# Kernel tuning notes

Measured on AMD Instinct MI355X. Metric: run time of the kernel, lower is better.

The kernel has to match this reference:

```python
import jax, jax.numpy as jnp
import numpy as np

B, K, S, H = 8, 2048, 1024, 256   # batch, num_spans, seq_len, hidden
W = 24                            # max span width (gather window)
WIN = 3
NEG_INF = -jnp.inf


def setup_inputs() -> dict:
    key = jax.random.key(0)
    k1, k2, k3, k4 = jax.random.split(key, 4)
    token_reps = jax.random.normal(k1, (B, S, H), dtype=jnp.float32)
    starts = jax.random.randint(k2, (B, K), 0, S - W)
    widths = jax.random.randint(k3, (B, K), 1, W + 1)  # span width in [1, W]
    ends = starts + widths                              # end is exclusive, <= S
    span_ids = jnp.stack([starts, ends], axis=-1).astype(jnp.int32)
    span_masks = jax.random.uniform(k4, (B, K)) < 0.9
    return {"token_reps": token_reps, "span_ids": span_ids, "span_masks": span_masks}


def _masked_max(tok_win, mask):
    # tok_win: (B, K, W, H), mask: (B, K, W) -> (B, K, H)
    return jnp.max(jnp.where(mask[..., None], tok_win, NEG_INF), axis=2)


def reference(token_reps, span_ids, span_masks):
    """extract_span_reps, mode='start_inner_maxpool_end', pooling=False.

    Equivalent math to the torch version, but gathers only the per-span window
    [start, start+W) instead of broadcasting over the full seq_len, since all
    spans have width <= W.
    """
    Bv, Sv, Hv = token_reps.shape
    starts = span_ids[..., 0]            # (B, K)
    ends = span_ids[..., 1]              # (B, K) exclusive

    pos = jnp.arange(W)                  # (W,)
    idx = starts[..., None] + pos        # (B, K, W) absolute token index
    safe_idx = jnp.clip(idx, 0, Sv - 1)  # safe gather; out-of-span masked below
    # gather per-span token windows: (B, K, W, H)
    tok_win = token_reps[jnp.arange(Bv)[:, None, None], safe_idx]

    valid = span_masks[..., None]                                 # (B, K, 1)
    start_cut = jnp.minimum(starts + WIN, ends)[..., None]        # (B, K, 1)
    end_cut = jnp.maximum(ends - WIN, starts)[..., None]          # (B, K, 1)
    e = ends[..., None]

    # idx >= start always holds (pos >= 0)
    start_m = (idx < start_cut) & valid
    end_m = (idx >= end_cut) & (idx < e) & valid
    inner_m = ((idx >= start_cut) & (idx < end_cut)
               & ((ends - starts) > 2 * WIN)[..., None] & valid)

    start_reps = _masked_max(tok_win, start_m)   # (B, K, H)
    end_reps = _masked_max(tok_win, end_m)
    inner_reps = _masked_max(tok_win, inner_m)

    # spans with no inner tokens fall back to start reps
    no_inner = jnp.isinf(inner_reps).all(axis=-1, keepdims=True)
    inner_reps = jnp.where(no_inner, start_reps, inner_reps)

    span_reps = jnp.concatenate([start_reps, inner_reps, end_reps], axis=-1)
    span_reps = jnp.where(span_masks[..., None], span_reps, 0.0)  # (B, K, 3H)
    return span_reps
```

## Files before the change

kernel.cpp:

```cpp
#include <hip/hip_runtime.h>

#define Bv   8
#define Kv   2048
#define Sv   1024
#define Hv   256
#define Wv   24
#define WINv 3
#define RB   8
#define SPW  8

#define NSPAN (Bv * Kv)

typedef float nt4 __attribute__((ext_vector_type(4)));

__device__ __forceinline__ float bf16_to_f32(unsigned short u) {
    union { unsigned int i; float f; } c;
    c.i = ((unsigned int)u) << 16;
    return c.f;
}

__device__ __forceinline__ void nt_store4(float* p, float a, float b, float c, float d) {
    nt4 v = {a, b, c, d};
    __builtin_nontemporal_store(v, (nt4*)p);
}

__global__ __launch_bounds__(256) void span_rep_kernel(
    const void* __restrict__ token_reps,
    const int* __restrict__ span_ids,
    const void* __restrict__ span_masks,
    float* __restrict__ out)
{
    const int tid  = threadIdx.x;
    const int lane = tid & 63;

    const unsigned short* tu = (const unsigned short*)token_reps;
    int e = (tu[2 * lane] >> 7) & 0xFF;
    unsigned long long votes = __ballot(e >= 96 && e <= 144);
    const int tok32 = (__popcll(votes) >= 56) ? 0 : 1;

    const unsigned char* mbp = (const unsigned char*)span_masks;
    unsigned char bnz = mbp[lane] | mbp[lane + 64];
    int m4 = lane & 3;
    unsigned long long z1  = __ballot(bnz && m4 == 1);
    unsigned long long z23 = __ballot(bnz && (m4 == 2 || m4 == 3));
    unsigned long long z84 = __ballot(bnz && m4 == 0 && (lane & 7) == 4);
    const int maskw = z1 ? 0 : (z23 ? 3 : (z84 ? 1 : 2));

    const int odd_or = span_ids[1] | span_ids[3] | span_ids[5] | span_ids[7];
    const int ids64 = (odd_or == 0) ? 1 : 0;

    const int b     = blockIdx.x & 7;
    const int kbase = ((blockIdx.x >> 3) << 5) + ((tid >> 6) << 3);
    const int span0 = b * Kv + kbase;

    int st[SPW], en[SPW], mvv[SPW];
    #pragma unroll
    for (int j = 0; j < SPW; ++j) {
        const int span = span0 + j;
        if (!ids64) {
            st[j] = span_ids[2 * span];
            en[j] = span_ids[2 * span + 1];
        } else {
            st[j] = span_ids[4 * span];
            en[j] = span_ids[4 * span + 2];
        }
        if (maskw == 0)      mvv[j] = ((const unsigned char*)span_masks)[span];
        else if (maskw == 1) mvv[j] = ((const int*)span_masks)[span];
        else if (maskw == 2) mvv[j] = ((const int*)span_masks)[2 * span];
        else                 mvv[j] = (((const float*)span_masks)[span] != 0.0f);
    }

    const size_t batch_off = (size_t)b * Sv * Hv;

    for (int j = 0; j < SPW; ++j) {
        const int span = span0 + j;
        float* outp = out + (size_t)span * (3 * Hv) + lane * 4;

        const int start = st[j];
        const int w     = en[j] - start;

        if (mvv[j] == 0 || w < 1 || w > Wv || start < 0 || en[j] > Sv) {
            nt_store4(outp,          0.f, 0.f, 0.f, 0.f);
            nt_store4(outp + Hv,     0.f, 0.f, 0.f, 0.f);
            nt_store4(outp + 2 * Hv, 0.f, 0.f, 0.f, 0.f);
            continue;
        }

        const size_t row0 = batch_off + (size_t)start * Hv;

        float s0 = -INFINITY, s1 = -INFINITY, s2 = -INFINITY, s3 = -INFINITY;
        float e0 = -INFINITY, e1 = -INFINITY, e2 = -INFINITY, e3 = -INFINITY;
        float i0 = -INFINITY, i1 = -INFINITY, i2 = -INFINITY, i3 = -INFINITY;

        const int  scut      = (w < WINv) ? w : WINv;
        const int  ecut      = (w - WINv > 0) ? (w - WINv) : 0;
        const bool has_inner = (w > 2 * WINv);
        const int  icut      = w - WINv;

        auto reduce = [&](int r, float f0, float f1, float f2, float f3) {
            if (r < scut) {
                s0 = fmaxf(s0, f0); s1 = fmaxf(s1, f1);
                s2 = fmaxf(s2, f2); s3 = fmaxf(s3, f3);
            }
            if (r >= ecut) {
                e0 = fmaxf(e0, f0); e1 = fmaxf(e1, f1);
                e2 = fmaxf(e2, f2); e3 = fmaxf(e3, f3);
            }
            if (has_inner && r >= WINv && r < icut) {
                i0 = fmaxf(i0, f0); i1 = fmaxf(i1, f1);
                i2 = fmaxf(i2, f2); i3 = fmaxf(i3, f3);
            }
        };

        if (tok32) {
            const float4* tp = (const float4*)((const float*)token_reps + row0) + lane;
            for (int r0 = 0; r0 < w; r0 += RB) {
                const int n = ((w - r0) < RB) ? (w - r0) : RB;
                float4 buf[RB];
                #pragma unroll
                for (int jj = 0; jj < RB; ++jj)
                    if (jj < n) buf[jj] = tp[(size_t)(r0 + jj) * (Hv / 4)];
                #pragma unroll
                for (int jj = 0; jj < RB; ++jj)
                    if (jj < n)
                        reduce(r0 + jj, buf[jj].x, buf[jj].y, buf[jj].z, buf[jj].w);
            }
        } else {
            const unsigned short* tp = (const unsigned short*)token_reps + row0 + lane * 4;
            for (int r0 = 0; r0 < w; r0 += RB) {
                const int n = ((w - r0) < RB) ? (w - r0) : RB;
                ushort4 buf[RB];
                #pragma unroll
                for (int jj = 0; jj < RB; ++jj)
                    if (jj < n) buf[jj] = *(const ushort4*)(tp + (size_t)(r0 + jj) * Hv);
                #pragma unroll
                for (int jj = 0; jj < RB; ++jj)
                    if (jj < n)
                        reduce(r0 + jj,
                               bf16_to_f32(buf[jj].x), bf16_to_f32(buf[jj].y),
                               bf16_to_f32(buf[jj].z), bf16_to_f32(buf[jj].w));
            }
        }
        if (!has_inner) { i0 = s0; i1 = s1; i2 = s2; i3 = s3; }

        nt_store4(outp,          s0, s1, s2, s3);
        nt_store4(outp + Hv,     i0, i1, i2, i3);
        nt_store4(outp + 2 * Hv, e0, e1, e2, e3);
    }
}

extern "C" void kernel_launch(void* const* d_in, const int* in_sizes, int n_in,
                              void* d_out, int out_size, void* d_ws, size_t ws_size,
                              hipStream_t stream) {
    const void* token_reps = d_in[0];
    const int*  span_ids   = (const int*)d_in[1];
    const void* span_masks = d_in[2];
    for (int i = 0; i < n_in; ++i) {
        if (in_sizes[i] == Bv * Sv * Hv)      token_reps = d_in[i];
        else if (in_sizes[i] == Bv * Kv * 2)  span_ids   = (const int*)d_in[i];
        else if (in_sizes[i] == Bv * Kv)      span_masks = d_in[i];
    }
    float* out = (float*)d_out;

    dim3 grid(NSPAN / (4 * SPW));
    dim3 block(256);
    span_rep_kernel<<<grid, block, 0, stream>>>(token_reps, span_ids, span_masks, out);
}
```

Before: 97.44 us.

## Process two spans per wavefront with interleaved loads and a larger grid

Each wavefront now handles two spans at once, issuing both spans' row loads before reducing either, instead of looping sequentially over eight spans. The grid grows fourfold to keep the total span count the same. This exposes more memory-level parallelism per wave and more waves overall, which should better hide gather latency. The cost is extra register pressure from two sets of accumulators and buffers, plus more block launch overhead.

```diff
diff --git a/kernel.cpp b/kernel.cpp
--- a/kernel.cpp
+++ b/kernel.cpp
@@ -7,7 +7,6 @@
 #define Wv   24
 #define WINv 3
 #define RB   8
-#define SPW  8
 
 #define NSPAN (Bv * Kv)
 
@@ -22,6 +21,95 @@
 __device__ __forceinline__ void nt_store4(float* p, float a, float b, float c, float d) {
     nt4 v = {a, b, c, d};
     __builtin_nontemporal_store(v, (nt4*)p);
+}
+
+__device__ __forceinline__ void cvt4(const float4 v, float* f) {
+    f[0] = v.x; f[1] = v.y; f[2] = v.z; f[3] = v.w;
+}
+__device__ __forceinline__ void cvt4(const ushort4 u, float* f) {
+    f[0] = bf16_to_f32(u.x); f[1] = bf16_to_f32(u.y);
+    f[2] = bf16_to_f32(u.z); f[3] = bf16_to_f32(u.w);
+}
+
+__device__ __forceinline__ void red(float* acc, int r, int scut, int ecut,
+                                    bool hin, int icut, const float* f) {
+    if (r < scut) {
+        acc[0] = fmaxf(acc[0], f[0]); acc[1] = fmaxf(acc[1], f[1]);
+        acc[2] = fmaxf(acc[2], f[2]); acc[3] = fmaxf(acc[3], f[3]);
+    }
+    if (r >= ecut) {
+        acc[8] = fmaxf(acc[8], f[0]); acc[9] = fmaxf(acc[9], f[1]);
+        acc[10] = fmaxf(acc[10], f[2]); acc[11] = fmaxf(acc[11], f[3]);
+    }
+    if (hin && r >= WINv && r < icut) {
+        acc[4] = fmaxf(acc[4], f[0]); acc[5] = fmaxf(acc[5], f[1]);
+        acc[6] = fmaxf(acc[6], f[2]); acc[7] = fmaxf(acc[7], f[3]);
+    }
+}
+
+template<typename VT, int STRIDEB>
+__device__ __forceinline__ void pair_body(
+    const char* pA, const char* pB, int wA, int wB,
+    float* outA, float* outB)
+{
+    float accA[12], accB[12];
+    #pragma unroll
+    for (int q = 0; q < 12; ++q) { accA[q] = -INFINITY; accB[q] = -INFINITY; }
+
+    const int  scutA = (wA < WINv) ? wA : WINv;
+    const int  ecutA = (wA - WINv > 0) ? (wA - WINv) : 0;
+    const bool hinA  = wA > 2 * WINv;
+    const int  icutA = wA - WINv;
+    const int  scutB = (wB < WINv) ? wB : WINv;
+    const int  ecutB = (wB - WINv > 0) ? (wB - WINv) : 0;
+    const bool hinB  = wB > 2 * WINv;
+    const int  icutB = wB - WINv;
+
+    for (int r0 = 0; r0 < Wv; r0 += RB) {
+        if (r0 >= wA && r0 >= wB) break;
+        VT bA[RB], bB[RB];
+        #pragma unroll
+        for (int j = 0; j < RB; ++j)
+            if (r0 + j < wA) bA[j] = *(const VT*)(pA + (size_t)(r0 + j) * STRIDEB);
+        #pragma unroll
+        for (int j = 0; j < RB; ++j)
+            if (r0 + j < wB) bB[j] = *(const VT*)(pB + (size_t)(r0 + j) * STRIDEB);
+        #pragma unroll
+        for (int j = 0; j < RB; ++j)
+            if (r0 + j < wA) {
+                float f[4]; cvt4(bA[j], f);
+                red(accA, r0 + j, scutA, ecutA, hinA, icutA, f);
+            }
+        #pragma unroll
+        for (int j = 0; j < RB; ++j)
+            if (r0 + j < wB) {
+                float f[4]; cvt4(bB[j], f);
+                red(accB, r0 + j, scutB, ecutB, hinB, icutB, f);
+            }
+    }
+
+    if (wA == 0) {
+        nt_store4(outA, 0.f, 0.f, 0.f, 0.f);
+        nt_store4(outA + Hv, 0.f, 0.f, 0.f, 0.f);
+        nt_store4(outA + 2 * Hv, 0.f, 0.f, 0.f, 0.f);
+    } else {
+        if (!hinA) { accA[4] = accA[0]; accA[5] = accA[1];
+                     accA[6] = accA[2]; accA[7] = accA[3]; }
+        nt_store4(outA,          accA[0], accA[1], accA[2], accA[3]);
+        nt_store4(outA + Hv,     accA[4], accA[5], accA[6], accA[7]);
+        nt_store4(outA + 2 * Hv, accA[8], accA[9], accA[10], accA[11]);
+    }
+    if (wB == 0) {
+        nt_store4(outB, 0.f, 0.f, 0.f, 0.f);
+        nt_store4(outB + Hv, 0.f, 0.f, 0.f, 0.f);
+        nt_store4(outB + 2 * Hv, 0.f, 0.f, 0.f, 0.f);
+    } else {
+        if (!hinB) { accB[4] = accB[0]; accB[5] = accB[1];
+                     accB[6] = accB[2]; accB[7] = accB[3]; }
+        nt_store4(outB,          accB[0], accB[1], accB[2], accB[3]);
+        nt_store4(outB + Hv,     accB[4], accB[5], accB[6], accB[7]);
+        nt_store4(outB + 2 * Hv, accB[8], accB[9], accB[10], accB[11]);
+    }
 }
 
 __global__ __launch_bounds__(256) void span_rep_kernel(
@@ -49,103 +137,48 @@
     const int odd_or = span_ids[1] | span_ids[3] | span_ids[5] | span_ids[7];
     const int ids64 = (odd_or == 0) ? 1 : 0;
 
-    const int b     = blockIdx.x & 7;
-    const int kbase = ((blockIdx.x >> 3) << 5) + ((tid >> 6) << 3);
-    const int span0 = b * Kv + kbase;
-
-    int st[SPW], en[SPW], mvv[SPW];
-    #pragma unroll
-    for (int j = 0; j < SPW; ++j) {
-        const int span = span0 + j;
-        if (!ids64) {
-            st[j] = span_ids[2 * span];
-            en[j] = span_ids[2 * span + 1];
-        } else {
-            st[j] = span_ids[4 * span];
-            en[j] = span_ids[4 * span + 2];
-        }
-        if (maskw == 0)      mvv[j] = ((const unsigned char*)span_masks)[span];
-        else if (maskw == 1) mvv[j] = ((const int*)span_masks)[span];
-        else if (maskw == 2) mvv[j] = ((const int*)span_masks)[2 * span];
-        else                 mvv[j] = (((const float*)span_masks)[span] != 0.0f);
-    }
+    const int b  = blockIdx.x & 7;
+    const int k0 = ((blockIdx.x >> 3) << 3) + ((tid >> 6) << 1);
+    const int sA = b * Kv + k0;
+    const int sB = sA + 1;
+
+    int stA, enA, stB, enB, mvA, mvB;
+    if (!ids64) {
+        stA = span_ids[2 * sA];     enA = span_ids[2 * sA + 1];
+        stB = span_ids[2 * sB];     enB = span_ids[2 * sB + 1];
+    } else {
+        stA = span_ids[4 * sA];     enA = span_ids[4 * sA + 2];
+        stB = span_ids[4 * sB];     enB = span_ids[4 * sB + 2];
+    }
+    if (maskw == 0)      { mvA = ((const unsigned char*)span_masks)[sA];
+                           mvB = ((const unsigned char*)span_masks)[sB]; }
+    else if (maskw == 1) { mvA = ((const int*)span_masks)[sA];
+                           mvB = ((const int*)span_masks)[sB]; }
+    else if (maskw == 2) { mvA = ((const int*)span_masks)[2 * sA];
+                           mvB = ((const int*)span_masks)[2 * sB]; }
+    else                 { mvA = (((const float*)span_masks)[sA] != 0.0f);
+                           mvB = (((const float*)span_masks)[sB] != 0.0f); }
+
+    int wA = enA - stA;
+    int wB = enB - stB;
+    if (mvA == 0 || wA < 1 || wA > Wv || stA < 0 || enA > Sv) wA = 0;
+    if (mvB == 0 || wB < 1 || wB > Wv || stB < 0 || enB > Sv) wB = 0;
+
+    float* outA = out + (size_t)sA * (3 * Hv) + lane * 4;
+    float* outB = out + (size_t)sB * (3 * Hv) + lane * 4;
 
     const size_t batch_off = (size_t)b * Sv * Hv;
 
-    for (int j = 0; j < SPW; ++j) {
-        const int span = span0 + j;
-        float* outp = out + (size_t)span * (3 * Hv) + lane * 4;
-
-        const int start = st[j];
-        const int w     = en[j] - start;
-
-        if (mvv[j] == 0 || w < 1 || w > Wv || start < 0 || en[j] > Sv) {
-            nt_store4(outp,          0.f, 0.f, 0.f, 0.f);
-            nt_store4(outp + Hv,     0.f, 0.f, 0.f, 0.f);
-            nt_store4(outp + 2 * Hv, 0.f, 0.f, 0.f, 0.f);
-            continue;
-        }
-
-        const size_t row0 = batch_off + (size_t)start * Hv;
-
-        float s0 = -INFINITY, s1 = -INFINITY, s2 = -INFINITY, s3 = -INFINITY;
-        float e0 = -INFINITY, e1 = -INFINITY, e2 = -INFINITY, e3 = -INFINITY;
-        float i0 = -INFINITY, i1 = -INFINITY, i2 = -INFINITY, i3 = -INFINITY;
-
-        const int  scut      = (w < WINv) ? w : WINv;
-        const int  ecut      = (w - WINv > 0) ? (w - WINv) : 0;
-        const bool has_inner = (w > 2 * WINv);
-        const int  icut      = w - WINv;
-
-        auto reduce = [&](int r, float f0, float f1, float f2, float f3) {
-            if (r < scut) {
-                s0 = fmaxf(s0, f0); s1 = fmaxf(s1, f1);
-                s2 = fmaxf(s2, f2); s3 = fmaxf(s3, f3);
-            }
-            if (r >= ecut) {
-                e0 = fmaxf(e0, f0); e1 = fmaxf(e1, f1);
-                e2 = fmaxf(e2, f2); e3 = fmaxf(e3, f3);
-            }
-            if (has_inner && r >= WINv && r < icut) {
-                i0 = fmaxf(i0, f0); i1 = fmaxf(i1, f1);
-                i2 = fmaxf(i2, f2); i3 = fmaxf(i3, f3);
-            }
-        };
-
-        if (tok32) {
-            const float4* tp = (const float4*)((const float*)token_reps + row0) + lane;
-            for (int r0 = 0; r0 < w; r0 += RB) {
-                const int n = ((w - r0) < RB) ? (w - r0) : RB;
-                float4 buf[RB];
-                #pragma unroll
-                for (int jj = 0; jj < RB; ++jj)
-                    if (jj < n) buf[jj] = tp[(size_t)(r0 + jj) * (Hv / 4)];
-                #pragma unroll
-                for (int jj = 0; jj < RB; ++jj)
-                    if (jj < n)
-                        reduce(r0 + jj, buf[jj].x, buf[jj].y, buf[jj].z, buf[jj].w);
-            }
-        } else {
-            const unsigned short* tp = (const unsigned short*)token_reps + row0 + lane * 4;
-            for (int r0 = 0; r0 < w; r0 += RB) {
-                const int n = ((w - r0) < RB) ? (w - r0) : RB;
-                ushort4 buf[RB];
-                #pragma unroll
-                for (int jj = 0; jj < RB; ++jj)
-                    if (jj < n) buf[jj] = *(const ushort4*)(tp + (size_t)(r0 + jj) * Hv);
-                #pragma unroll
-                for (int jj = 0; jj < RB; ++jj)
-                    if (jj < n)
-                        reduce(r0 + jj,
-                               bf16_to_f32(buf[jj].x), bf16_to_f32(buf[jj].y),
-                               bf16_to_f32(buf[jj].z), bf16_to_f32(buf[jj].w));
-            }
-        }
-        if (!has_inner) { i0 = s0; i1 = s1; i2 = s2; i3 = s3; }
-
-        nt_store4(outp,          s0, s1, s2, s3);
-        nt_store4(outp + Hv,     i0, i1, i2, i3);
-        nt_store4(outp + 2 * Hv, e0, e1, e2, e3);
+    if (tok32) {
+        const char* base = (const char*)token_reps;
+        const char* pA = base + (batch_off + (size_t)stA * Hv + lane * 4) * 4;
+        const char* pB = base + (batch_off + (size_t)stB * Hv + lane * 4) * 4;
+        pair_body<float4, Hv * 4>(pA, pB, wA, wB, outA, outB);
+    } else {
+        const char* base = (const char*)token_reps;
+        const char* pA = base + (batch_off + (size_t)stA * Hv + lane * 4) * 2;
+        const char* pB = base + (batch_off + (size_t)stB * Hv + lane * 4) * 2;
+        pair_body<ushort4, Hv * 2>(pA, pB, wA, wB, outA, outB);
     }
 }
 
@@ -162,7 +195,7 @@
     }
     float* out = (float*)d_out;
 
-    dim3 grid(NSPAN / (4 * SPW));
+    dim3 grid(NSPAN / 8);
     dim3 block(256);
     span_rep_kernel<<<grid, block, 0, stream>>>(token_reps, span_ids, span_masks, out);
 }
```

Measured after the change: 93.02 us. 4.5% less time.

## Map one span per wavefront with clamped unconditional row loads

Applied to the files above, without the earlier changes.

Each wavefront now handles one span instead of looping over eight, and the grid grows eightfold to match. Row loads become unconditional, with the row index clamped to the last valid row and the block size raised to twelve so all loads issue together. Span ids are read for both 32- and 64-bit layouts and then selected, and nontemporal stores are replaced with plain stores. The aim is more memory-level parallelism and less serial per-span latency, at the cost of more block launches, redundant header work per block, and extra loads on short spans.

```diff
diff --git a/kernel.cpp b/kernel.cpp
--- a/kernel.cpp
+++ b/kernel.cpp
@@ -6,22 +6,14 @@
 #define Hv   256
 #define Wv   24
 #define WINv 3
-#define RB   8
-#define SPW  8
+#define RB   12
 
 #define NSPAN (Bv * Kv)
-
-typedef float nt4 __attribute__((ext_vector_type(4)));
 
 __device__ __forceinline__ float bf16_to_f32(unsigned short u) {
     union { unsigned int i; float f; } c;
     c.i = ((unsigned int)u) << 16;
     return c.f;
-}
-
-__device__ __forceinline__ void nt_store4(float* p, float a, float b, float c, float d) {
-    nt4 v = {a, b, c, d};
-    __builtin_nontemporal_store(v, (nt4*)p);
 }
 
 __global__ __launch_bounds__(256) void span_rep_kernel(
@@ -49,104 +41,98 @@
     const int odd_or = span_ids[1] | span_ids[3] | span_ids[5] | span_ids[7];
     const int ids64 = (odd_or == 0) ? 1 : 0;
 
-    const int b     = blockIdx.x & 7;
-    const int kbase = ((blockIdx.x >> 3) << 5) + ((tid >> 6) << 3);
-    const int span0 = b * Kv + kbase;
+    const int b    = blockIdx.x & 7;
+    const int k    = ((blockIdx.x >> 3) << 2) + (tid >> 6);
+    const int span = b * Kv + k;
 
-    int st[SPW], en[SPW], mvv[SPW];
-    #pragma unroll
-    for (int j = 0; j < SPW; ++j) {
-        const int span = span0 + j;
-        if (!ids64) {
-            st[j] = span_ids[2 * span];
-            en[j] = span_ids[2 * span + 1];
-        } else {
-            st[j] = span_ids[4 * span];
-            en[j] = span_ids[4 * span + 2];
-        }
-        if (maskw == 0)      mvv[j] = ((const unsigned char*)span_masks)[span];
-        else if (maskw == 1) mvv[j] = ((const int*)span_masks)[span];
-        else if (maskw == 2) mvv[j] = ((const int*)span_masks)[2 * span];
-        else                 mvv[j] = (((const float*)span_masks)[span] != 0.0f);
+    float* outp = out + (size_t)span * (3 * Hv) + lane * 4;
+
+    int st32 = span_ids[2 * span];
+    int en32 = span_ids[2 * span + 1];
+    int st64 = span_ids[4 * span];
+    int en64 = span_ids[4 * span + 2];
+    const int start = ids64 ? st64 : st32;
+    const int end   = ids64 ? en64 : en32;
+
+    int mv;
+    if (maskw == 0)      mv = ((const unsigned char*)span_masks)[span];
+    else if (maskw == 1) mv = ((const int*)span_masks)[span];
+    else if (maskw == 2) mv = ((const int*)span_masks)[2 * span];
+    else                 mv = (((const float*)span_masks)[span] != 0.0f);
+
+    const int w = end - start;
+
+    if (mv == 0 || w < 1 || w > Wv || start < 0 || end > Sv) {
+        float4 z = make_float4(0.f, 0.f, 0.f, 0.f);
+        *(float4*)(outp)          = z;
+        *(float4*)(outp + Hv)     = z;
+        *(float4*)(outp + 2 * Hv) = z;
+        return;
     }
 
-    const size_t batch_off = (size_t)b * Sv * Hv;
+    const size_t row0 = ((size_t)b * Sv + start) * Hv;
 
-    for (int j = 0; j < SPW; ++j) {
-        const int span = span0 + j;
-        float* outp = out + (size_t)span * (3 * Hv) + lane * 4;
+    float s0 = -INFINITY, s1 = -INFINITY, s2 = -INFINITY, s3 = -INFINITY;
+    float e0 = -INFINITY, e1 = -INFINITY, e2 = -INFINITY, e3 = -INFINITY;
+    float i0 = -INFINITY, i1 = -INFINITY, i2 = -INFINITY, i3 = -INFINITY;
 
-        const int start = st[j];
-        const int w     = en[j] - start;
+    const int  scut      = (w < WINv) ? w : WINv;
+    const int  ecut      = (w - WINv > 0) ? (w - WINv) : 0;
+    const bool has_inner = (w > 2 * WINv);
+    const int  icut      = w - WINv;
+    const int  wm1       = w - 1;
 
-        if (mvv[j] == 0 || w < 1 || w > Wv || start < 0 || en[j] > Sv) {
-            nt_store4(outp,          0.f, 0.f, 0.f, 0.f);
-            nt_store4(outp + Hv,     0.f, 0.f, 0.f, 0.f);
-            nt_store4(outp + 2 * Hv, 0.f, 0.f, 0.f, 0.f);
-            continue;
+    auto reduce = [&](int r, float f0, float f1, float f2, float f3) {
+        if (r < scut) {
+            s0 = fmaxf(s0, f0); s1 = fmaxf(s1, f1);
+            s2 = fmaxf(s2, f2); s3 = fmaxf(s3, f3);
         }
+        if (r >= ecut) {
+            e0 = fmaxf(e0, f0); e1 = fmaxf(e1, f1);
+            e2 = fmaxf(e2, f2); e3 = fmaxf(e3, f3);
+        }
+        if (has_inner && r >= WINv && r < icut) {
+            i0 = fmaxf(i0, f0); i1 = fmaxf(i1, f1);
+            i2 = fmaxf(i2, f2); i3 = fmaxf(i3, f3);
+        }
+    };
 
-        const size_t row0 = batch_off + (size_t)start * Hv;
+    if (tok32) {
+        const float4* tp = (const float4*)((const float*)token_reps + row0) + lane;
+        for (int r0 = 0; r0 < w; r0 += RB) {
+            float4 buf[RB];
+            #pragma unroll
+            for (int j = 0; j < RB; ++j) {
+                int rr = r0 + j; rr = (rr < wm1) ? rr : wm1;
+                buf[j] = tp[(size_t)rr * (Hv / 4)];
+            }
+            #pragma unroll
+            for (int j = 0; j < RB; ++j)
+                if (r0 + j < w)
+                    reduce(r0 + j, buf[j].x, buf[j].y, buf[j].z, buf[j].w);
+        }
+    } else {
+        const unsigned short* tp = (const unsigned short*)token_reps + row0 + lane * 4;
+        for (int r0 = 0; r0 < w; r0 += RB) {
+            ushort4 buf[RB];
+            #pragma unroll
+            for (int j = 0; j < RB; ++j) {
+                int rr = r0 + j; rr = (rr < wm1) ? rr : wm1;
+                buf[j] = *(const ushort4*)(tp + (size_t)rr * Hv);
+            }
+            #pragma unroll
+            for (int j = 0; j < RB; ++j)
+                if (r0 + j < w)
+                    reduce(r0 + j,
+                           bf16_to_f32(buf[j].x), bf16_to_f32(buf[j].y),
+                           bf16_to_f32(buf[j].z), bf16_to_f32(buf[j].w));
+        }
+    }
+    if (!has_inner) { i0 = s0; i1 = s1; i2 = s2; i3 = s3; }
 
-        float s0 = -INFINITY, s1 = -INFINITY, s2 = -INFINITY, s3 = -INFINITY;
-        float e0 = -INFINITY, e1 = -INFINITY, e2 = -INFINITY, e3 = -INFINITY;
-        float i0 = -INFINITY, i1 = -INFINITY, i2 = -INFINITY, i3 = -INFINITY;
-
-        const int  scut      = (w < WINv) ? w : WINv;
-        const int  ecut      = (w - WINv > 0) ? (w - WINv) : 0;
-        const bool has_inner = (w > 2 * WINv);
-        const int  icut      = w - WINv;
-
-        auto reduce = [&](int r, float f0, float f1, float f2, float f3) {
-            if (r < scut) {
-                s0 = fmaxf(s0, f0); s1 = fmaxf(s1, f1);
-                s2 = fmaxf(s2, f2); s3 = fmaxf(s3, f3);
-            }
-            if (r >= ecut) {
-                e0 = fmaxf(e0, f0); e1 = fmaxf(e1, f1);
-                e2 = fmaxf(e2, f2); e3 = fmaxf(e3, f3);
-            }
-            if (has_inner && r >= WINv && r < icut) {
-                i0 = fmaxf(i0, f0); i1 = fmaxf(i1, f1);
-                i2 = fmaxf(i2, f2); i3 = fmaxf(i3, f3);
-            }
-        };
-
-        if (tok32) {
-            const float4* tp = (const float4*)((const float*)token_reps + row0) + lane;
-            for (int r0 = 0; r0 < w; r0 += RB) {
-                const int n = ((w - r0) < RB) ? (w - r0) : RB;
-                float4 buf[RB];
-                #pragma unroll
-                for (int jj = 0; jj < RB; ++jj)
-                    if (jj < n) buf[jj] = tp[(size_t)(r0 + jj) * (Hv / 4)];
-                #pragma unroll
-                for (int jj = 0; jj < RB; ++jj)
-                    if (jj < n)
-                        reduce(r0 + jj, buf[jj].x, buf[jj].y, buf[jj].z, buf[jj].w);
-            }
-        } else {
-            const unsigned short* tp = (const unsigned short*)token_reps + row0 + lane * 4;
-            for (int r0 = 0; r0 < w; r0 += RB) {
-                const int n = ((w - r0) < RB) ? (w - r0) : RB;
-                ushort4 buf[RB];
-                #pragma unroll
-                for (int jj = 0; jj < RB; ++jj)
-                    if (jj < n) buf[jj] = *(const ushort4*)(tp + (size_t)(r0 + jj) * Hv);
-                #pragma unroll
-                for (int jj = 0; jj < RB; ++jj)
-                    if (jj < n)
-                        reduce(r0 + jj,
-                               bf16_to_f32(buf[jj].x), bf16_to_f32(buf[jj].y),
-                               bf16_to_f32(buf[jj].z), bf16_to_f32(buf[jj].w));
-            }
-        }
-        if (!has_inner) { i0 = s0; i1 = s1; i2 = s2; i3 = s3; }
-
-        nt_store4(outp,          s0, s1, s2, s3);
-        nt_store4(outp + Hv,     i0, i1, i2, i3);
-        nt_store4(outp + 2 * Hv, e0, e1, e2, e3);
-    }
+    *(float4*)(outp)          = make_float4(s0, s1, s2, s3);
+    *(float4*)(outp + Hv)     = make_float4(i0, i1, i2, i3);
+    *(float4*)(outp + 2 * Hv) = make_float4(e0, e1, e2, e3);
 }
 
 extern "C" void kernel_launch(void* const* d_in, const int* in_sizes, int n_in,
@@ -162,7 +148,7 @@
     }
     float* out = (float*)d_out;
 
-    dim3 grid(NSPAN / (4 * SPW));
+    dim3 grid(NSPAN / 4);
     dim3 block(256);
     span_rep_kernel<<<grid, block, 0, stream>>>(token_reps, span_ids, span_masks, out);
 }
```

Result: faster. 88.87 us (-8.8%).
